# Kernel optimization log

Hardware: AMD Instinct MI355X
Metric: run time of the kernel (lower is better)

The kernel has to match this reference:

```python
import jax, jax.numpy as jnp
import numpy as np

B = 65536          # batch
H_DIM, W_DIM = 8, 8  # feather_size tuple
N = H_DIM * W_DIM    # 64 flat features
INNER = (N + 1) ** 2 # 4225 = outer-product size after prepending ones column
EPS = 1e-6


def setup_inputs() -> dict:
    key = jax.random.key(0)
    k1, k2 = jax.random.split(key, 2)
    x = jax.random.normal(k1, (B, N), jnp.float32)
    # nn.Linear(INNER, N): weight [out, in] = [N, INNER]
    W = jax.random.normal(k2, (N, INNER), jnp.float32) / np.sqrt(INNER)
    b = jnp.zeros((N,), jnp.float32)
    gamma = jnp.ones((N,), jnp.float32)   # LayerNorm scale
    beta = jnp.zeros((N,), jnp.float32)   # LayerNorm shift
    return {"x": x, "W": W, "b": b, "gamma": gamma, "beta": beta}


def reference(x, W, b, gamma, beta):
    Bsz = x.shape[0]
    # prepend ones column: [B, N+1]
    ones = jnp.ones((Bsz, 1), x.dtype)
    x1 = jnp.concatenate([ones, x], axis=-1)
    # bmm outer product x1 @ x1^T per row -> [B, N+1, N+1], flatten to [B, INNER]
    outer = (x1[:, :, None] * x1[:, None, :]).reshape(Bsz, INNER)
    # Linear(INNER -> N)
    y = outer @ W.T + b  # [B, N]
    # UER-py LayerNorm: gamma*(y-u)/sqrt(var+eps)+beta over last dim
    u = jnp.mean(y, axis=-1, keepdims=True)
    s = jnp.mean((y - u) ** 2, axis=-1, keepdims=True)
    y = gamma * (y - u) / jnp.sqrt(s + EPS) + beta
    # final view back to the (out) feather matrix shape
    return y.reshape(Bsz, H_DIM, W_DIM)
```

## Files before the change

kernel.cpp:

```cpp
#include <hip/hip_runtime.h>
#include <stdint.h>
#include <stddef.h>

typedef _Float16 f16;
typedef _Float16 f16x2 __attribute__((ext_vector_type(2)));
typedef _Float16 f16x4 __attribute__((ext_vector_type(4)));
typedef _Float16 f16x8 __attribute__((ext_vector_type(8)));
typedef float f32x4 __attribute__((ext_vector_type(4)));

#define INNER_SZ 4225
#define WK 4224
#define KQ 4096

__global__ __launch_bounds__(256) void cm_prep(const float* __restrict__ W,
                                               const float* __restrict__ bias,
                                               f16* __restrict__ Wf,
                                               float* __restrict__ cvec) {
  int idx = blockIdx.x * 256 + threadIdx.x;
  if (idx < 64 * WK) {
    int o = idx / WK;
    int k = idx - o * WK;
    float v;
    if (k < KQ) {
      int i = k >> 6, j = k & 63;
      v = W[o * INNER_SZ + (i + 1) * 65 + (j + 1)];
    } else if (k < KQ + 64) {
      int j = k - KQ;
      v = W[o * INNER_SZ + (j + 1)] + W[o * INNER_SZ + (j + 1) * 65];
    } else {
      v = 0.f;
    }
    Wf[idx] = (f16)v;
  }
  if (idx < 64) cvec[idx] = W[idx * INNER_SZ] + bias[idx];
}

__device__ inline void gload_lds16(const void* g, void* l) {
  __builtin_amdgcn_global_load_lds(
      (const __attribute__((address_space(1))) uint32_t*)(uintptr_t)g,
      (__attribute__((address_space(3))) uint32_t*)(uintptr_t)l, 16, 0, 0);
}

__global__ __launch_bounds__(256, 2) void cm_main(
    const float* __restrict__ x, const f16* __restrict__ Wf,
    const float* __restrict__ cvec, const float* __restrict__ gamma,
    const float* __restrict__ beta, float* __restrict__ out) {
  __shared__ __align__(16) f16 xs[128 * 72];
  __shared__ __align__(16) f16 wlds[2][64 * 128];
  __shared__ float part[2][128][2];

  const int tid = threadIdx.x;
  const int lane = tid & 63;
  const int wid = tid >> 6;
  const int mg = wid & 1;
  const int ng = wid >> 1;
  const int g = lane >> 4;
  const int c15 = lane & 15;
  const int mbase = blockIdx.x * 128;

  {
#pragma unroll
    for (int jj = 0; jj < 4; ++jj) {
      int j = wid * 4 + jj;
      int cl = j * 4 + g;
      int soff = (c15 * 16) ^ ((cl & 7) << 4);
      gload_lds16(Wf + (size_t)cl * WK + (soff >> 1), &wlds[0][j * 512]);
    }
  }

#pragma unroll
  for (int it = 0; it < 8; ++it) {
    int off = it * 1024 + tid * 4;
    int row = off >> 6;
    int col = off & 63;
    const float4 v = *(const float4*)(x + (size_t)(mbase + row) * 64 + col);
    f16x4 h = {(f16)v.x, (f16)v.y, (f16)v.z, (f16)v.w};
    *(f16x4*)(xs + row * 72 + col) = h;
  }
  __syncthreads();

  f16x8 xjv[4][2];
#pragma unroll
  for (int mf = 0; mf < 4; ++mf) {
    int row = mg * 64 + mf * 16 + c15;
#pragma unroll
    for (int p = 0; p < 2; ++p)
      xjv[mf][p] = *(const f16x8*)(xs + row * 72 + p * 32 + g * 8);
  }

  f32x4 acc[4][2];
#pragma unroll
  for (int mf = 0; mf < 4; ++mf)
#pragma unroll
    for (int nf = 0; nf < 2; ++nf)
      acc[mf][nf] = (f32x4){0.f, 0.f, 0.f, 0.f};

  for (int t = 0; t < 32; ++t) {
    {
      int bi = (t + 1) & 1;
#pragma unroll
      for (int jj = 0; jj < 4; ++jj) {
        int j = wid * 4 + jj;
        int cl = j * 4 + g;
        int soff = (c15 * 16) ^ ((cl & 7) << 4);
        gload_lds16(Wf + (size_t)cl * WK + (t + 1) * 128 + (soff >> 1),
                    &wlds[bi][j * 512]);
      }
    }
    f16x2 xi2[4];
#pragma unroll
    for (int mf = 0; mf < 4; ++mf) {
      int row = mg * 64 + mf * 16 + c15;
      xi2[mf] = *(const f16x2*)(xs + row * 72 + 2 * t);
    }
    const char* wb = (const char*)&wlds[t & 1][0];
#pragma unroll
    for (int s = 0; s < 4; ++s) {
      f16x8 bf[2];
#pragma unroll
      for (int nf = 0; nf < 2; ++nf) {
        int col = ng * 32 + nf * 16 + c15;
        int kb = s * 64 + g * 16;
        bf[nf] = *(const f16x8*)(wb + col * 256 + (kb ^ ((c15 & 7) << 4)));
      }
#pragma unroll
      for (int mf = 0; mf < 4; ++mf) {
        f16 xv = xi2[mf][s >> 1];
        f16x8 xi8 = {xv, xv, xv, xv, xv, xv, xv, xv};
        f16x8 a = xi8 * xjv[mf][s & 1];
        acc[mf][0] = __builtin_amdgcn_mfma_f32_16x16x32_f16(a, bf[0], acc[mf][0], 0, 0, 0);
        acc[mf][1] = __builtin_amdgcn_mfma_f32_16x16x32_f16(a, bf[1], acc[mf][1], 0, 0, 0);
      }
    }
    __syncthreads();
  }

  {
    const char* wb = (const char*)&wlds[0][0];
#pragma unroll
    for (int s = 0; s < 2; ++s) {
      f16x8 bf[2];
#pragma unroll
      for (int nf = 0; nf < 2; ++nf) {
        int col = ng * 32 + nf * 16 + c15;
        int kb = s * 64 + g * 16;
        bf[nf] = *(const f16x8*)(wb + col * 256 + (kb ^ ((c15 & 7) << 4)));
      }
#pragma unroll
      for (int mf = 0; mf < 4; ++mf) {
        f16x8 a = xjv[mf][s];
        acc[mf][0] = __builtin_amdgcn_mfma_f32_16x16x32_f16(a, bf[0], acc[mf][0], 0, 0, 0);
        acc[mf][1] = __builtin_amdgcn_mfma_f32_16x16x32_f16(a, bf[1], acc[mf][1], 0, 0, 0);
      }
    }
  }

  float cv[2], gv[2], bv[2];
#pragma unroll
  for (int nf = 0; nf < 2; ++nf) {
    int col = ng * 32 + nf * 16 + c15;
    cv[nf] = cvec[col];
    gv[nf] = gamma[col];
    bv[nf] = beta[col];
  }
  float yv[4][2][4];
#pragma unroll
  for (int mf = 0; mf < 4; ++mf)
#pragma unroll
    for (int nf = 0; nf < 2; ++nf)
#pragma unroll
      for (int r = 0; r < 4; ++r)
        yv[mf][nf][r] = acc[mf][nf][r] + cv[nf];

#pragma unroll
  for (int mf = 0; mf < 4; ++mf) {
#pragma unroll
    for (int r = 0; r < 4; ++r) {
      float s = yv[mf][0][r] + yv[mf][1][r];
      float q = yv[mf][0][r] * yv[mf][0][r] + yv[mf][1][r] * yv[mf][1][r];
#pragma unroll
      for (int m = 1; m <= 8; m <<= 1) {
        s += __shfl_xor(s, m);
        q += __shfl_xor(q, m);
      }
      if (c15 == 0) {
        int lr = mg * 64 + mf * 16 + g * 4 + r;
        part[ng][lr][0] = s;
        part[ng][lr][1] = q;
      }
    }
  }
  __syncthreads();
#pragma unroll
  for (int mf = 0; mf < 4; ++mf) {
#pragma unroll
    for (int r = 0; r < 4; ++r) {
      int lr = mg * 64 + mf * 16 + g * 4 + r;
      float s = part[0][lr][0] + part[1][lr][0];
      float q = part[0][lr][1] + part[1][lr][1];
      float mean = s * 0.015625f;
      float var = q * 0.015625f - mean * mean;
      float rstd = rsqrtf(var + 1e-6f);
#pragma unroll
      for (int nf = 0; nf < 2; ++nf) {
        int col = ng * 32 + nf * 16 + c15;
        out[(size_t)(mbase + lr) * 64 + col] =
            gv[nf] * (yv[mf][nf][r] - mean) * rstd + bv[nf];
      }
    }
  }
}

extern "C" void kernel_launch(void* const* d_in, const int* in_sizes, int n_in,
                              void* d_out, int out_size, void* d_ws, size_t ws_size,
                              hipStream_t stream) {
  const float* x     = (const float*)d_in[0];
  const float* W     = (const float*)d_in[1];
  const float* bias  = (const float*)d_in[2];
  const float* gamma = (const float*)d_in[3];
  const float* beta  = (const float*)d_in[4];
  float* out = (float*)d_out;

  f16* Wf = (f16*)d_ws;
  float* cvec = (float*)((char*)d_ws + 64 * WK * 2);

  cm_prep<<<(64 * WK + 255) / 256, 256, 0, stream>>>(W, bias, Wf, cvec);
  cm_main<<<512, 256, 0, stream>>>(x, Wf, cvec, gamma, beta, out);
}
```

Before: 46.53 us.

## Give each wave its own W slice with triple-buffered per-wave loads

The warp layout changes from a 2x2 M/N split to four waves that each own 16 output columns across all 128 rows. Each wave stages only its own W columns into a private triple-buffered LDS region and waits with s_waitcnt vmcnt, so the per-iteration __syncthreads is gone. This removes block-wide barriers from the K loop and lets loads run two chunks ahead. In exchange each wave keeps more x fragments in registers (8 row fragments), and the LayerNorm reduction now combines four partial sums, reusing the xs buffer as scratch.

New measurement: 56.52 us. 1.21x slower.

```diff
diff --git a/kernel.cpp b/kernel.cpp
--- a/kernel.cpp
+++ b/kernel.cpp
@@ -46,27 +46,46 @@
     const float* __restrict__ cvec, const float* __restrict__ gamma,
     const float* __restrict__ beta, float* __restrict__ out) {
   __shared__ __align__(16) f16 xs[128 * 72];
-  __shared__ __align__(16) f16 wlds[2][64 * 128];
-  __shared__ float part[2][128][2];
+  __shared__ __align__(16) f16 wbuf[4][3][2048];
 
   const int tid = threadIdx.x;
   const int lane = tid & 63;
-  const int wid = tid >> 6;
-  const int mg = wid & 1;
-  const int ng = wid >> 1;
+  const int w = tid >> 6;
   const int g = lane >> 4;
   const int c15 = lane & 15;
+  const int w16 = w * 16;
+  const int swz = (c15 & 7) << 4;
   const int mbase = blockIdx.x * 128;
 
-  {
-#pragma unroll
-    for (int jj = 0; jj < 4; ++jj) {
-      int j = wid * 4 + jj;
-      int cl = j * 4 + g;
-      int soff = (c15 * 16) ^ ((cl & 7) << 4);
-      gload_lds16(Wf + (size_t)cl * WK + (soff >> 1), &wlds[0][j * 512]);
-    }
-  }
+#define STAGE_CHUNK(T, BI)                                                 \
+  _Pragma("unroll") for (int jj = 0; jj < 4; ++jj) {                       \
+    int cl = 4 * jj + g;                                                   \
+    int soff = (c15 * 8) ^ ((cl & 7) << 3);   \
+    gload_lds16(Wf + (size_t)(w16 + cl) * WK + (T) * 128 + soff,           \
+                &wbuf[w][BI][jj * 512]);                                   \
+  }
+
+#define QUAD_CHUNK(T, BI)                                                  \
+  {                                                                        \
+    f16x2 xi2[8];                                                          \
+    _Pragma("unroll") for (int mf = 0; mf < 8; ++mf)                       \
+        xi2[mf] = *(const f16x2*)(xs + (mf * 16 + c15) * 72 + 2 * (T));    \
+    const char* wb = (const char*)&wbuf[w][BI][0];                         \
+    _Pragma("unroll") for (int s = 0; s < 4; ++s) {                        \
+      f16x8 bf = *(const f16x8*)(wb + c15 * 256 +                          \
+                                 ((s * 64 + g * 16) ^ swz));               \
+      _Pragma("unroll") for (int mf = 0; mf < 8; ++mf) {                   \
+        f16 xv = xi2[mf][(s >> 1)];                                        \
+        f16x8 xi8 = {xv, xv, xv, xv, xv, xv, xv, xv};                      \
+        f16x8 a = xi8 * xjv[mf][s & 1];                                    \
+        acc[mf] = __builtin_amdgcn_mfma_f32_16x16x32_f16(a, bf, acc[mf],   \
+                                                         0, 0, 0);         \
+      }                                                                    \
+    }                                                                      \
+  }
+
+  STAGE_CHUNK(0, 0);
+  STAGE_CHUNK(1, 1);
 
 #pragma unroll
   for (int it = 0; it < 8; ++it) {
@@ -79,136 +98,94 @@
   }
   __syncthreads();
 
-  f16x8 xjv[4][2];
-#pragma unroll
-  for (int mf = 0; mf < 4; ++mf) {
-    int row = mg * 64 + mf * 16 + c15;
+  f16x8 xjv[8][2];
+#pragma unroll
+  for (int mf = 0; mf < 8; ++mf) {
+    int row = mf * 16 + c15;
 #pragma unroll
     for (int p = 0; p < 2; ++p)
       xjv[mf][p] = *(const f16x8*)(xs + row * 72 + p * 32 + g * 8);
   }
 
-  f32x4 acc[4][2];
-#pragma unroll
-  for (int mf = 0; mf < 4; ++mf)
-#pragma unroll
-    for (int nf = 0; nf < 2; ++nf)
-      acc[mf][nf] = (f32x4){0.f, 0.f, 0.f, 0.f};
-
-  for (int t = 0; t < 32; ++t) {
-    {
-      int bi = (t + 1) & 1;
-#pragma unroll
-      for (int jj = 0; jj < 4; ++jj) {
-        int j = wid * 4 + jj;
-        int cl = j * 4 + g;
-        int soff = (c15 * 16) ^ ((cl & 7) << 4);
-        gload_lds16(Wf + (size_t)cl * WK + (t + 1) * 128 + (soff >> 1),
-                    &wlds[bi][j * 512]);
+  f32x4 acc[8];
+#pragma unroll
+  for (int mf = 0; mf < 8; ++mf) acc[mf] = (f32x4){0.f, 0.f, 0.f, 0.f};
+
+  int bc = 0, bs = 2;
+  for (int t = 0; t < 31; ++t) {
+    STAGE_CHUNK(t + 2, bs);
+    asm volatile("s_waitcnt vmcnt(8)" ::: "memory");
+    QUAD_CHUNK(t, bc);
+    bc = (bc == 2) ? 0 : bc + 1;
+    bs = (bs == 2) ? 0 : bs + 1;
+  }
+  asm volatile("s_waitcnt vmcnt(4)" ::: "memory");
+  QUAD_CHUNK(31, bc);
+  bc = (bc == 2) ? 0 : bc + 1;
+  asm volatile("s_waitcnt vmcnt(0)" ::: "memory");
+  {
+    const char* wb = (const char*)&wbuf[w][bc][0];
+#pragma unroll
+    for (int s = 0; s < 2; ++s) {
+      f16x8 bf = *(const f16x8*)(wb + c15 * 256 + ((s * 64 + g * 16) ^ swz));
+#pragma unroll
+      for (int mf = 0; mf < 8; ++mf) {
+        f16x8 a = xjv[mf][s];
+        acc[mf] = __builtin_amdgcn_mfma_f32_16x16x32_f16(a, bf, acc[mf], 0, 0, 0);
       }
     }
-    f16x2 xi2[4];
-#pragma unroll
-    for (int mf = 0; mf < 4; ++mf) {
-      int row = mg * 64 + mf * 16 + c15;
-      xi2[mf] = *(const f16x2*)(xs + row * 72 + 2 * t);
-    }
-    const char* wb = (const char*)&wlds[t & 1][0];
-#pragma unroll
-    for (int s = 0; s < 4; ++s) {
-      f16x8 bf[2];
-#pragma unroll
-      for (int nf = 0; nf < 2; ++nf) {
-        int col = ng * 32 + nf * 16 + c15;
-        int kb = s * 64 + g * 16;
-        bf[nf] = *(const f16x8*)(wb + col * 256 + (kb ^ ((c15 & 7) << 4)));
-      }
-#pragma unroll
-      for (int mf = 0; mf < 4; ++mf) {
-        f16 xv = xi2[mf][s >> 1];
-        f16x8 xi8 = {xv, xv, xv, xv, xv, xv, xv, xv};
-        f16x8 a = xi8 * xjv[mf][s & 1];
-        acc[mf][0] = __builtin_amdgcn_mfma_f32_16x16x32_f16(a, bf[0], acc[mf][0], 0, 0, 0);
-        acc[mf][1] = __builtin_amdgcn_mfma_f32_16x16x32_f16(a, bf[1], acc[mf][1], 0, 0, 0);
-      }
-    }
-    __syncthreads();
-  }
-
-  {
-    const char* wb = (const char*)&wlds[0][0];
-#pragma unroll
-    for (int s = 0; s < 2; ++s) {
-      f16x8 bf[2];
-#pragma unroll
-      for (int nf = 0; nf < 2; ++nf) {
-        int col = ng * 32 + nf * 16 + c15;
-        int kb = s * 64 + g * 16;
-        bf[nf] = *(const f16x8*)(wb + col * 256 + (kb ^ ((c15 & 7) << 4)));
-      }
-#pragma unroll
-      for (int mf = 0; mf < 4; ++mf) {
-        f16x8 a = xjv[mf][s];
-        acc[mf][0] = __builtin_amdgcn_mfma_f32_16x16x32_f16(a, bf[0], acc[mf][0], 0, 0, 0);
-        acc[mf][1] = __builtin_amdgcn_mfma_f32_16x16x32_f16(a, bf[1], acc[mf][1], 0, 0, 0);
-      }
-    }
-  }
-
-  float cv[2], gv[2], bv[2];
-#pragma unroll
-  for (int nf = 0; nf < 2; ++nf) {
-    int col = ng * 32 + nf * 16 + c15;
-    cv[nf] = cvec[col];
-    gv[nf] = gamma[col];
-    bv[nf] = beta[col];
-  }
-  float yv[4][2][4];
-#pragma unroll
-  for (int mf = 0; mf < 4; ++mf)
-#pragma unroll
-    for (int nf = 0; nf < 2; ++nf)
-#pragma unroll
-      for (int r = 0; r < 4; ++r)
-        yv[mf][nf][r] = acc[mf][nf][r] + cv[nf];
-
-#pragma unroll
-  for (int mf = 0; mf < 4; ++mf) {
+  }
+
+  const float cv = cvec[w16 + c15];
+  const float gv = gamma[w16 + c15];
+  const float bv = beta[w16 + c15];
+
+  float yv[8][4];
+#pragma unroll
+  for (int mf = 0; mf < 8; ++mf)
+#pragma unroll
+    for (int r = 0; r < 4; ++r) yv[mf][r] = acc[mf][r] + cv;
+
+  __syncthreads();
+  float* part = (float*)xs;
+
+#pragma unroll
+  for (int mf = 0; mf < 8; ++mf) {
 #pragma unroll
     for (int r = 0; r < 4; ++r) {
-      float s = yv[mf][0][r] + yv[mf][1][r];
-      float q = yv[mf][0][r] * yv[mf][0][r] + yv[mf][1][r] * yv[mf][1][r];
+      float s = yv[mf][r];
+      float q = yv[mf][r] * yv[mf][r];
 #pragma unroll
       for (int m = 1; m <= 8; m <<= 1) {
         s += __shfl_xor(s, m);
         q += __shfl_xor(q, m);
       }
       if (c15 == 0) {
-        int lr = mg * 64 + mf * 16 + g * 4 + r;
-        part[ng][lr][0] = s;
-        part[ng][lr][1] = q;
+        int row = mf * 16 + g * 4 + r;
+        part[(w * 128 + row) * 2 + 0] = s;
+        part[(w * 128 + row) * 2 + 1] = q;
       }
     }
   }
   __syncthreads();
 #pragma unroll
-  for (int mf = 0; mf < 4; ++mf) {
+  for (int mf = 0; mf < 8; ++mf) {
 #pragma unroll
     for (int r = 0; r < 4; ++r) {
-      int lr = mg * 64 + mf * 16 + g * 4 + r;
-      float s = part[0][lr][0] + part[1][lr][0];
-      float q = part[0][lr][1] + part[1][lr][1];
+      int row = mf * 16 + g * 4 + r;
+      float s = part[row * 2 + 0] + part[(128 + row) * 2 + 0] +
+                part[(256 + row) * 2 + 0] + part[(384 + row) * 2 + 0];
+      float q = part[row * 2 + 1] + part[(128 + row) * 2 + 1] +
+                part[(256 + row) * 2 + 1] + part[(384 + row) * 2 + 1];
       float mean = s * 0.015625f;
       float var = q * 0.015625f - mean * mean;
       float rstd = rsqrtf(var + 1e-6f);
-#pragma unroll
-      for (int nf = 0; nf < 2; ++nf) {
-        int col = ng * 32 + nf * 16 + c15;
-        out[(size_t)(mbase + lr) * 64 + col] =
-            gv[nf] * (yv[mf][nf][r] - mean) * rstd + bv[nf];
-      }
-    }
-  }
+      out[(size_t)(mbase + row) * 64 + w16 + c15] =
+          gv * (yv[mf][r] - mean) * rstd + bv;
+    }
+  }
+#undef STAGE_CHUNK
+#undef QUAD_CHUNK
 }
 
 extern "C" void kernel_launch(void* const* d_in, const int* in_sizes, int n_in,
```

## Deepen W staging to a four-buffer ring with counted waits and occupancy three

Applied to the files above, without the earlier changes.

The K loop now runs in 64-wide chunks (64 iterations) over a 4-slot LDS ring, staged two chunks ahead. A per-iteration __syncthreads is replaced by s_waitcnt vmcnt plus s_barrier with raised priority around the MFMA section. LDS use drops (the part buffer now reuses xs) and launch bounds move to 3 blocks per CU. The A operand scaling now uses packed f16x2 multiplies. More iterations mean more barriers, and the handwritten vmcnt counts must match the number of outstanding loads exactly.

Measured after the change: 48.92 us. +5.1%, slower.

```diff
diff --git a/kernel.cpp b/kernel.cpp
--- a/kernel.cpp
+++ b/kernel.cpp
@@ -11,6 +11,7 @@
 #define INNER_SZ 4225
 #define WK 4224
 #define KQ 4096
+#define XSTR 72
 
 __global__ __launch_bounds__(256) void cm_prep(const float* __restrict__ W,
                                                const float* __restrict__ bias,
@@ -41,32 +42,36 @@
       (__attribute__((address_space(3))) uint32_t*)(uintptr_t)l, 16, 0, 0);
 }
 
-__global__ __launch_bounds__(256, 2) void cm_main(
+__global__ __launch_bounds__(256, 3) void cm_main(
     const float* __restrict__ x, const f16* __restrict__ Wf,
     const float* __restrict__ cvec, const float* __restrict__ gamma,
     const float* __restrict__ beta, float* __restrict__ out) {
-  __shared__ __align__(16) f16 xs[128 * 72];
-  __shared__ __align__(16) f16 wlds[2][64 * 128];
-  __shared__ float part[2][128][2];
+  __shared__ __align__(16) f16 xs[128 * XSTR];
+  __shared__ __align__(16) f16 wbuf[4][4096];
 
   const int tid = threadIdx.x;
   const int lane = tid & 63;
-  const int wid = tid >> 6;
-  const int mg = wid & 1;
-  const int ng = wid >> 1;
+  const int w = tid >> 6;
   const int g = lane >> 4;
   const int c15 = lane & 15;
+  const int mg = w & 1;
+  const int ng = w >> 1;
+  const int swz = (c15 & 7) << 4;
   const int mbase = blockIdx.x * 128;
 
-  {
-#pragma unroll
-    for (int jj = 0; jj < 4; ++jj) {
-      int j = wid * 4 + jj;
-      int cl = j * 4 + g;
-      int soff = (c15 * 16) ^ ((cl & 7) << 4);
-      gload_lds16(Wf + (size_t)cl * WK + (soff >> 1), &wlds[0][j * 512]);
-    }
-  }
+  const int scol0 = 16 * w + (lane >> 3);
+  const int sgran = ((lane & 7) ^ (lane >> 3)) * 8;
+
+#define STAGE(T, S)                                                       \
+  do {                                                                    \
+    gload_lds16(Wf + (size_t)scol0 * WK + (T) * 64 + sgran,               \
+                &wbuf[S][(2 * w) * 512]);                                 \
+    gload_lds16(Wf + (size_t)(scol0 + 8) * WK + (T) * 64 + sgran,         \
+                &wbuf[S][(2 * w + 1) * 512]);                             \
+  } while (0)
+
+  STAGE(0, 0);
+  STAGE(1, 1);
 
 #pragma unroll
   for (int it = 0; it < 8; ++it) {
@@ -75,7 +80,7 @@
     int col = off & 63;
     const float4 v = *(const float4*)(x + (size_t)(mbase + row) * 64 + col);
     f16x4 h = {(f16)v.x, (f16)v.y, (f16)v.z, (f16)v.w};
-    *(f16x4*)(xs + row * 72 + col) = h;
+    *(f16x4*)(xs + row * XSTR + col) = h;
   }
   __syncthreads();
 
@@ -84,8 +89,8 @@
   for (int mf = 0; mf < 4; ++mf) {
     int row = mg * 64 + mf * 16 + c15;
 #pragma unroll
-    for (int p = 0; p < 2; ++p)
-      xjv[mf][p] = *(const f16x8*)(xs + row * 72 + p * 32 + g * 8);
+    for (int s = 0; s < 2; ++s)
+      xjv[mf][s] = *(const f16x8*)(xs + row * XSTR + s * 32 + g * 8);
   }
 
   f32x4 acc[4][2];
@@ -95,98 +100,96 @@
     for (int nf = 0; nf < 2; ++nf)
       acc[mf][nf] = (f32x4){0.f, 0.f, 0.f, 0.f};
 
-  for (int t = 0; t < 32; ++t) {
-    {
-      int bi = (t + 1) & 1;
-#pragma unroll
-      for (int jj = 0; jj < 4; ++jj) {
-        int j = wid * 4 + jj;
-        int cl = j * 4 + g;
-        int soff = (c15 * 16) ^ ((cl & 7) << 4);
-        gload_lds16(Wf + (size_t)cl * WK + (t + 1) * 128 + (soff >> 1),
-                    &wlds[bi][j * 512]);
-      }
-    }
-    f16x2 xi2[4];
+  auto quad = [&](int T, int S) {
+    uint32_t sp[4];
 #pragma unroll
     for (int mf = 0; mf < 4; ++mf) {
       int row = mg * 64 + mf * 16 + c15;
-      xi2[mf] = *(const f16x2*)(xs + row * 72 + 2 * t);
-    }
-    const char* wb = (const char*)&wlds[t & 1][0];
-#pragma unroll
-    for (int s = 0; s < 4; ++s) {
-      f16x8 bf[2];
-#pragma unroll
-      for (int nf = 0; nf < 2; ++nf) {
-        int col = ng * 32 + nf * 16 + c15;
-        int kb = s * 64 + g * 16;
-        bf[nf] = *(const f16x8*)(wb + col * 256 + (kb ^ ((c15 & 7) << 4)));
-      }
+      uint32_t u = *(const uint16_t*)(xs + row * XSTR + T);
+      sp[mf] = u | (u << 16);
+    }
+    const char* wb = (const char*)&wbuf[S][0];
+#pragma unroll
+    for (int s = 0; s < 2; ++s) {
+      const int ko = (s * 64 + g * 16) ^ swz;
+      f16x8 bf0 = *(const f16x8*)(wb + (ng * 32 + c15) * 128 + ko);
+      f16x8 bf1 = *(const f16x8*)(wb + (ng * 32 + 16 + c15) * 128 + ko);
 #pragma unroll
       for (int mf = 0; mf < 4; ++mf) {
-        f16 xv = xi2[mf][s >> 1];
-        f16x8 xi8 = {xv, xv, xv, xv, xv, xv, xv, xv};
-        f16x8 a = xi8 * xjv[mf][s & 1];
-        acc[mf][0] = __builtin_amdgcn_mfma_f32_16x16x32_f16(a, bf[0], acc[mf][0], 0, 0, 0);
-        acc[mf][1] = __builtin_amdgcn_mfma_f32_16x16x32_f16(a, bf[1], acc[mf][1], 0, 0, 0);
-      }
-    }
-    __syncthreads();
-  }
-
+        f16x2 spv = __builtin_bit_cast(f16x2, sp[mf]);
+        f16x8 xv = xjv[mf][s];
+        f16x8 a;
+#pragma unroll
+        for (int e = 0; e < 4; ++e)
+          ((f16x2*)&a)[e] = spv * ((f16x2*)&xv)[e];
+        acc[mf][0] = __builtin_amdgcn_mfma_f32_16x16x32_f16(a, bf0, acc[mf][0], 0, 0, 0);
+        acc[mf][1] = __builtin_amdgcn_mfma_f32_16x16x32_f16(a, bf1, acc[mf][1], 0, 0, 0);
+      }
+    }
+  };
+
+  for (int t = 0; t < 63; ++t) {
+    STAGE(t + 2, (t + 2) & 3);
+    asm volatile("s_waitcnt vmcnt(4)" ::: "memory");
+    __builtin_amdgcn_s_barrier();
+    __builtin_amdgcn_s_setprio(1);
+    quad(t, t & 3);
+    __builtin_amdgcn_s_setprio(0);
+  }
+  asm volatile("s_waitcnt vmcnt(2)" ::: "memory");
+  __builtin_amdgcn_s_barrier();
+  __builtin_amdgcn_s_setprio(1);
+  quad(63, 63 & 3);
+  __builtin_amdgcn_s_setprio(0);
+  asm volatile("s_waitcnt vmcnt(0)" ::: "memory");
+  __builtin_amdgcn_s_barrier();
   {
-    const char* wb = (const char*)&wlds[0][0];
+    const char* wb = (const char*)&wbuf[0][0];
 #pragma unroll
     for (int s = 0; s < 2; ++s) {
-      f16x8 bf[2];
-#pragma unroll
-      for (int nf = 0; nf < 2; ++nf) {
-        int col = ng * 32 + nf * 16 + c15;
-        int kb = s * 64 + g * 16;
-        bf[nf] = *(const f16x8*)(wb + col * 256 + (kb ^ ((c15 & 7) << 4)));
-      }
+      const int ko = (s * 64 + g * 16) ^ swz;
+      f16x8 bf0 = *(const f16x8*)(wb + (ng * 32 + c15) * 128 + ko);
+      f16x8 bf1 = *(const f16x8*)(wb + (ng * 32 + 16 + c15) * 128 + ko);
 #pragma unroll
       for (int mf = 0; mf < 4; ++mf) {
         f16x8 a = xjv[mf][s];
-        acc[mf][0] = __builtin_amdgcn_mfma_f32_16x16x32_f16(a, bf[0], acc[mf][0], 0, 0, 0);
-        acc[mf][1] = __builtin_amdgcn_mfma_f32_16x16x32_f16(a, bf[1], acc[mf][1], 0, 0, 0);
-      }
-    }
-  }
-
-  float cv[2], gv[2], bv[2];
-#pragma unroll
-  for (int nf = 0; nf < 2; ++nf) {
-    int col = ng * 32 + nf * 16 + c15;
-    cv[nf] = cvec[col];
-    gv[nf] = gamma[col];
-    bv[nf] = beta[col];
-  }
+        acc[mf][0] = __builtin_amdgcn_mfma_f32_16x16x32_f16(a, bf0, acc[mf][0], 0, 0, 0);
+        acc[mf][1] = __builtin_amdgcn_mfma_f32_16x16x32_f16(a, bf1, acc[mf][1], 0, 0, 0);
+      }
+    }
+  }
+
+  const float cv0 = cvec[ng * 32 + c15],      cv1 = cvec[ng * 32 + 16 + c15];
+  const float gv0 = gamma[ng * 32 + c15],     gv1 = gamma[ng * 32 + 16 + c15];
+  const float bv0 = beta[ng * 32 + c15],      bv1 = beta[ng * 32 + 16 + c15];
+
   float yv[4][2][4];
 #pragma unroll
   for (int mf = 0; mf < 4; ++mf)
 #pragma unroll
-    for (int nf = 0; nf < 2; ++nf)
-#pragma unroll
-      for (int r = 0; r < 4; ++r)
-        yv[mf][nf][r] = acc[mf][nf][r] + cv[nf];
+    for (int r = 0; r < 4; ++r) {
+      yv[mf][0][r] = acc[mf][0][r] + cv0;
+      yv[mf][1][r] = acc[mf][1][r] + cv1;
+    }
+
+  __syncthreads();
+  float* part = (float*)xs;
 
 #pragma unroll
   for (int mf = 0; mf < 4; ++mf) {
 #pragma unroll
     for (int r = 0; r < 4; ++r) {
-      float s = yv[mf][0][r] + yv[mf][1][r];
-      float q = yv[mf][0][r] * yv[mf][0][r] + yv[mf][1][r] * yv[mf][1][r];
+      float s2 = yv[mf][0][r] + yv[mf][1][r];
+      float q2 = yv[mf][0][r] * yv[mf][0][r] + yv[mf][1][r] * yv[mf][1][r];
 #pragma unroll
       for (int m = 1; m <= 8; m <<= 1) {
-        s += __shfl_xor(s, m);
-        q += __shfl_xor(q, m);
+        s2 += __shfl_xor(s2, m);
+        q2 += __shfl_xor(q2, m);
       }
       if (c15 == 0) {
-        int lr = mg * 64 + mf * 16 + g * 4 + r;
-        part[ng][lr][0] = s;
-        part[ng][lr][1] = q;
+        int row = mg * 64 + mf * 16 + g * 4 + r;
+        part[(ng * 128 + row) * 2 + 0] = s2;
+        part[(ng * 128 + row) * 2 + 1] = q2;
       }
     }
   }
@@ -195,20 +198,19 @@
   for (int mf = 0; mf < 4; ++mf) {
 #pragma unroll
     for (int r = 0; r < 4; ++r) {
-      int lr = mg * 64 + mf * 16 + g * 4 + r;
-      float s = part[0][lr][0] + part[1][lr][0];
-      float q = part[0][lr][1] + part[1][lr][1];
-      float mean = s * 0.015625f;
-      float var = q * 0.015625f - mean * mean;
+      int row = mg * 64 + mf * 16 + g * 4 + r;
+      float s2 = part[row * 2 + 0] + part[(128 + row) * 2 + 0];
+      float q2 = part[row * 2 + 1] + part[(128 + row) * 2 + 1];
+      float mean = s2 * 0.015625f;
+      float var = q2 * 0.015625f - mean * mean;
       float rstd = rsqrtf(var + 1e-6f);
-#pragma unroll
-      for (int nf = 0; nf < 2; ++nf) {
-        int col = ng * 32 + nf * 16 + c15;
-        out[(size_t)(mbase + lr) * 64 + col] =
-            gv[nf] * (yv[mf][nf][r] - mean) * rstd + bv[nf];
-      }
-    }
-  }
+      out[(size_t)(mbase + row) * 64 + ng * 32 + c15] =
+          gv0 * (yv[mf][0][r] - mean) * rstd + bv0;
+      out[(size_t)(mbase + row) * 64 + ng * 32 + 16 + c15] =
+          gv1 * (yv[mf][1][r] - mean) * rstd + bv1;
+    }
+  }
+#undef STAGE
 }
 
 extern "C" void kernel_launch(void* const* d_in, const int* in_sizes, int n_in,
```
